# Kernel optimization log

Hardware: AMD Instinct MI355X
Metric: run time of the kernel (lower is better)

The kernel has to match this reference:

```python
import jax, jax.numpy as jnp
import numpy as np

DIM = 1024
DEPTH = 4
VOCAB = 32000
B, N = 2, 2048
DFF = 4096
FG = 0.9  # frac_gradient_state_transition


def setup_inputs() -> dict:
    key = jax.random.key(0)
    ks = jax.random.split(key, 12)
    s = 0.02
    d = DIM
    return {
        "tokens": jax.random.randint(ks[0], (B, N), 0, VOCAB, dtype=jnp.int32),
        "emb": jax.random.normal(ks[1], (VOCAB, d), jnp.float32) * s,
        "g1": jnp.ones((DEPTH, d), jnp.float32),
        "Wqkv": jax.random.normal(ks[2], (DEPTH, d, 3 * d), jnp.float32) * s,
        "Wa": jax.random.normal(ks[3], (DEPTH, d, 2 * d), jnp.float32) * s,
        "ba": jnp.zeros((DEPTH, 2 * d), jnp.float32),
        "Wg": jax.random.normal(ks[4], (DEPTH, d, d), jnp.float32) * s,
        "Wo": jax.random.normal(ks[5], (DEPTH, d, d), jnp.float32) * s,
        "g2": jnp.ones((DEPTH, d), jnp.float32),
        "W1": jax.random.normal(ks[6], (DEPTH, d, DFF), jnp.float32) * s,
        "b1": jnp.zeros((DEPTH, DFF), jnp.float32),
        "W2": jax.random.normal(ks[7], (DEPTH, DFF, d), jnp.float32) * s,
        "b2": jnp.zeros((DEPTH, d), jnp.float32),
        "gf": jnp.ones((d,), jnp.float32),
        "Wl": jax.random.normal(ks[8], (d, VOCAB), jnp.float32) * s,
    }


def _rms(x, g):
    # F.normalize(x, dim=-1) * sqrt(dim) * gamma  (eps=1e-12 like torch)
    nrm = jnp.sqrt(jnp.sum(x * x, axis=-1, keepdims=True))
    return x / jnp.maximum(nrm, 1e-12) * (x.shape[-1] ** 0.5) * g


def _gate_loop(q, k, v, a):
    # q,k,v: (BH, n, 1) real; a: (BH, n, 1) complex
    kv = k[..., :, None] * v[..., None, :]          # (BH, n, 1, 1)
    a = a[..., None]                                 # (BH, n, 1, 1)
    a = jax.nn.sigmoid(jnp.abs(a)) * jnp.exp(1j * jnp.angle(a))  # polar(sigmoid(|a|), angle(a))

    def binop(c1, c2):
        a_i, kv_i = c1
        a_j, kv_j = c2
        return a_j * a_i, a_j.real * kv_i + kv_j

    _, kv = jax.lax.associative_scan(binop, (a, kv), axis=1)
    return jnp.einsum('bnd,bnde->bne', q, kv)        # (BH, n, 1)


def _attn(x, g1, Wqkv, Wa, ba, Wg, Wo):
    b, n, d = x.shape
    h = d  # heads == dim_inner, head dim == 1
    xn = _rms(x, g1)
    q, k, v = jnp.split(xn @ Wqkv, 3, axis=-1)       # each (b, n, d)
    split = lambda t: t.reshape(b, n, h, 1).transpose(0, 2, 1, 3).reshape(b * h, n, 1)
    q, k, v = split(q), split(k), split(v)
    al = (xn @ Wa + ba).reshape(b, n, h, 2).transpose(0, 2, 1, 3).reshape(b * h, n, 1, 2)
    a = al[..., 0] + 1j * al[..., 1]                 # (b*h, n, 1) complex
    a = FG * a + (1.0 - FG) * jax.lax.stop_gradient(a)
    out = _gate_loop(q, k, v, a)                     # (b*h, n, 1)
    out = out.reshape(b, h, n, 1).transpose(0, 2, 1, 3).reshape(b, n, d)
    gates = jax.nn.silu(xn @ Wg)
    return (gates * out) @ Wo


def _ff(x, g2, W1, b1, W2, b2):
    hdn = jax.nn.gelu(_rms(x, g2) @ W1 + b1, approximate=False)
    return hdn @ W2 + b2


def reference(tokens, emb, g1, Wqkv, Wa, ba, Wg, Wo, g2, W1, b1, W2, b2, gf, Wl):
    x = emb[tokens]                                  # (B, N, DIM)
    for i in range(DEPTH):
        x = x + _attn(x, g1[i], Wqkv[i], Wa[i], ba[i], Wg[i], Wo[i])
        x = x + _ff(x, g2[i], W1[i], b1[i], W2[i], b2[i])
    return _rms(x, gf) @ Wl                          # (B, N, VOCAB) logits
```

## Files before the change

### kernel.cpp

```cpp
#include <hip/hip_runtime.h>


typedef float fx4 __attribute__((ext_vector_type(4)));
typedef _Float16 f16x8 __attribute__((ext_vector_type(8)));
typedef _Float16 f16x4 __attribute__((ext_vector_type(4)));

#define AS1 __attribute__((address_space(1)))
#define AS3 __attribute__((address_space(3)))

__global__ __launch_bounds__(256) void transpose_f16_kernel(
    const float* __restrict__ in, _Float16* __restrict__ out,
    int K, int N, size_t ostride)
{
    __shared__ float tile[32][33];
    const int b = blockIdx.z;
    in  += (size_t)b * K * N;
    out += (size_t)b * ostride;
    const int k0 = blockIdx.x * 32, n0 = blockIdx.y * 32;
    const int tr = threadIdx.x >> 3;
    const int tc = (threadIdx.x & 7) * 4;
    fx4 v = *(const fx4*)&in[(size_t)(k0 + tr) * N + n0 + tc];
    tile[tr][tc + 0] = v[0]; tile[tr][tc + 1] = v[1];
    tile[tr][tc + 2] = v[2]; tile[tr][tc + 3] = v[3];
    __syncthreads();
    f16x4 o;
    #pragma unroll
    for (int e = 0; e < 4; ++e) o[e] = (_Float16)tile[tc + e][tr];
    *(f16x4*)&out[(size_t)(n0 + tr) * K + k0 + tc] = o;
}

__device__ __forceinline__ float row_rms_scale(float ss) {
    #pragma unroll
    for (int off = 32; off > 0; off >>= 1) ss += __shfl_down(ss, off, 64);
    __shared__ float wsum[4];
    if ((threadIdx.x & 63) == 0) wsum[threadIdx.x >> 6] = ss;
    __syncthreads();
    const float nrm = sqrtf(wsum[0] + wsum[1] + wsum[2] + wsum[3]);
    return 32.0f / fmaxf(nrm, 1e-12f);
}

__global__ __launch_bounds__(256) void embed_rms_kernel(
    const int* __restrict__ tokens, const float* __restrict__ emb,
    const float* __restrict__ g, float* __restrict__ x, _Float16* __restrict__ xn)
{
    const int row = blockIdx.x;
    const int t = tokens[row];
    const int c = threadIdx.x * 4;
    fx4 v = *(const fx4*)&emb[(size_t)t * 1024 + c];
    *(fx4*)&x[(size_t)row * 1024 + c] = v;
    const float scale = row_rms_scale(v[0]*v[0] + v[1]*v[1] + v[2]*v[2] + v[3]*v[3]);
    fx4 gg = *(const fx4*)&g[c];
    f16x4 o;
    #pragma unroll
    for (int e = 0; e < 4; ++e) o[e] = (_Float16)(v[e] * scale * gg[e]);
    *(f16x4*)&xn[(size_t)row * 1024 + c] = o;
}

__global__ __launch_bounds__(256) void rms_f16_kernel(
    const float* __restrict__ x, const float* __restrict__ g,
    _Float16* __restrict__ outh)
{
    const int row = blockIdx.x;
    const int c = threadIdx.x * 4;
    fx4 v = *(const fx4*)&x[(size_t)row * 1024 + c];
    const float scale = row_rms_scale(v[0]*v[0] + v[1]*v[1] + v[2]*v[2] + v[3]*v[3]);
    fx4 gg = *(const fx4*)&g[c];
    f16x4 o;
    #pragma unroll
    for (int e = 0; e < 4; ++e) o[e] = (_Float16)(v[e] * scale * gg[e]);
    *(f16x4*)&outh[(size_t)row * 1024 + c] = o;
}

__global__ __launch_bounds__(256) void prep_qkv_kernel(
    const float* __restrict__ qkv, float* __restrict__ qT, float* __restrict__ kvT)
{
    __shared__ float tq[32][33], tkv[32][33];
    const int n0 = blockIdx.x * 32, h0 = blockIdx.y * 32, b = blockIdx.z;
    const int tr = threadIdx.x >> 3;
    const int tc = (threadIdx.x & 7) * 4;
    const float* row = qkv + ((size_t)b * 2048 + n0 + tr) * 3072;
    fx4 qv = *(const fx4*)&row[h0 + tc];
    fx4 kv = *(const fx4*)&row[1024 + h0 + tc];
    fx4 vv = *(const fx4*)&row[2048 + h0 + tc];
    #pragma unroll
    for (int e = 0; e < 4; ++e) { tq[tr][tc + e] = qv[e]; tkv[tr][tc + e] = kv[e] * vv[e]; }
    __syncthreads();
    fx4 oq, okv;
    #pragma unroll
    for (int e = 0; e < 4; ++e) { oq[e] = tq[tc + e][tr]; okv[e] = tkv[tc + e][tr]; }
    const size_t ob = ((size_t)b * 1024 + h0 + tr) * 2048 + n0 + tc;
    *(fx4*)&qT[ob] = oq;
    *(fx4*)&kvT[ob] = okv;
}

__global__ __launch_bounds__(256) void prep_a_kernel(
    const float* __restrict__ al, float* __restrict__ aReT, float* __restrict__ aImT)
{
    __shared__ float tre[32][33], tim[32][33];
    const int n0 = blockIdx.x * 32, h0 = blockIdx.y * 32, b = blockIdx.z;
    const int tr = threadIdx.x >> 3;
    const int tcf = (threadIdx.x & 7) * 8;
    const float* row = al + ((size_t)b * 2048 + n0 + tr) * 2048 + 2 * h0;
    fx4 v0 = *(const fx4*)&row[tcf];
    fx4 v1 = *(const fx4*)&row[tcf + 4];
    #pragma unroll
    for (int p = 0; p < 4; ++p) {
        float re = (p < 2) ? v0[2 * p] : v1[2 * (p - 2)];
        float im = (p < 2) ? v0[2 * p + 1] : v1[2 * (p - 2) + 1];
        float r = sqrtf(re * re + im * im);
        float sg = 1.0f / (1.0f + expf(-r));
        float a_re, a_im;
        if (r > 0.0f) { float inv = sg / r; a_re = re * inv; a_im = im * inv; }
        else          { a_re = sg; a_im = 0.0f; }
        tre[tr][tcf / 2 + p] = a_re;
        tim[tr][tcf / 2 + p] = a_im;
    }
    __syncthreads();
    const int tc = (threadIdx.x & 7) * 4;
    fx4 ore, oim;
    #pragma unroll
    for (int e = 0; e < 4; ++e) { ore[e] = tre[tc + e][tr]; oim[e] = tim[tc + e][tr]; }
    const size_t ob = ((size_t)b * 1024 + h0 + tr) * 2048 + n0 + tc;
    *(fx4*)&aReT[ob] = ore;
    *(fx4*)&aImT[ob] = oim;
}

__device__ __forceinline__ int pidx(int i) { return i + (i >> 5); }

__global__ __launch_bounds__(256) void scanT_kernel(
    const float* __restrict__ kvT, const float* __restrict__ aReT,
    const float* __restrict__ aImT, const float* __restrict__ qT,
    float* __restrict__ yT)
{
    const int tid = threadIdx.x;
    const size_t base = (size_t)blockIdx.x * 2048;
    __shared__ float s_re[2048 + 64], s_im[2048 + 64], s_kv[2048 + 64];

    for (int i = tid; i < 512; i += 256) {
        fx4 kv = *(const fx4*)&kvT[base + i * 4];
        fx4 re = *(const fx4*)&aReT[base + i * 4];
        fx4 im = *(const fx4*)&aImT[base + i * 4];
        #pragma unroll
        for (int e = 0; e < 4; ++e) {
            const int j = pidx(i * 4 + e);
            s_kv[j] = kv[e]; s_re[j] = re[e]; s_im[j] = im[e];
        }
    }
    __syncthreads();

    for (int d = 0; d < 11; ++d) {
        const int half = 1 << d, stride = half << 1;
        const int npairs = 2048 >> (d + 1);
        for (int i = tid; i < npairs; i += 256) {
            const int rj = pidx(i * stride + stride - 1);
            const int lj = pidx(i * stride + stride - 1 - half);
            float lre = s_re[lj], lim = s_im[lj], lkv = s_kv[lj];
            float rre = s_re[rj], rim = s_im[rj], rkv = s_kv[rj];
            s_kv[rj] = rre * lkv + rkv;
            s_re[rj] = rre * lre - rim * lim;
            s_im[rj] = rre * lim + rim * lre;
        }
        __syncthreads();
    }
    for (int d = 9; d >= 0; --d) {
        const int w = 1 << d;
        const int nupd = (2048 >> (d + 1)) - 1;
        for (int t = tid; t < nupd; t += 256) {
            const int i = t + 1;
            const int rj = pidx((2 * i + 1) * w - 1);
            const int lj = pidx(2 * i * w - 1);
            float lre = s_re[lj], lim = s_im[lj], lkv = s_kv[lj];
            float rre = s_re[rj], rim = s_im[rj], rkv = s_kv[rj];
            s_kv[rj] = rre * lkv + rkv;
            s_re[rj] = rre * lre - rim * lim;
            s_im[rj] = rre * lim + rim * lre;
        }
        __syncthreads();
    }
    for (int i = tid; i < 512; i += 256) {
        fx4 q = *(const fx4*)&qT[base + i * 4];
        fx4 o;
        #pragma unroll
        for (int e = 0; e < 4; ++e) o[e] = q[e] * s_kv[pidx(i * 4 + e)];
        *(fx4*)&yT[base + i * 4] = o;
    }
}

__global__ __launch_bounds__(256) void gate_kernel(
    const float* __restrict__ G, const float* __restrict__ yT,
    _Float16* __restrict__ gated)
{
    __shared__ float ty[32][33];
    const int n0 = blockIdx.x * 32, h0 = blockIdx.y * 32, b = blockIdx.z;
    const int tr = threadIdx.x >> 3;
    const int tc = (threadIdx.x & 7) * 4;
    fx4 yv = *(const fx4*)&yT[((size_t)b * 1024 + h0 + tr) * 2048 + n0 + tc];
    #pragma unroll
    for (int e = 0; e < 4; ++e) ty[tr][tc + e] = yv[e];
    __syncthreads();
    const size_t grow = ((size_t)b * 2048 + n0 + tr) * 1024 + h0 + tc;
    fx4 gv = *(const fx4*)&G[grow];
    f16x4 o;
    #pragma unroll
    for (int e = 0; e < 4; ++e) {
        const float s = gv[e] / (1.0f + expf(-gv[e]));
        o[e] = (_Float16)(s * ty[tc + e][tr]);
    }
    *(f16x4*)&gated[grow] = o;
}

__global__ __launch_bounds__(256) void combine2_rms_kernel(
    const float* __restrict__ p, const float* __restrict__ bias,
    const float* __restrict__ g, float* __restrict__ x, _Float16* __restrict__ xn)
{
    const int row = blockIdx.x;
    const int c = threadIdx.x * 4;
    const size_t i = (size_t)row * 1024 + c;
    fx4 a = *(const fx4*)&p[i];
    fx4 b = *(const fx4*)&p[i + (size_t)4096 * 1024];
    fx4 xx = *(const fx4*)&x[i];
    fx4 bb = *(const fx4*)&bias[c];
    fx4 o;
    #pragma unroll
    for (int e = 0; e < 4; ++e) o[e] = xx[e] + (a[e] + b[e] + bb[e]);
    *(fx4*)&x[i] = o;
    const float scale = row_rms_scale(o[0]*o[0] + o[1]*o[1] + o[2]*o[2] + o[3]*o[3]);
    fx4 gg = *(const fx4*)&g[c];
    f16x4 oh;
    #pragma unroll
    for (int e = 0; e < 4; ++e) oh[e] = (_Float16)(o[e] * scale * gg[e]);
    *(f16x4*)&xn[i] = oh;
}

template<int EPI, int BM, int BN, int WTM>
__global__ __launch_bounds__((BM / WTM) * (BN / 64) * 64) void gemm_kernel(
    const _Float16* __restrict__ A, const _Float16* __restrict__ Bt,
    const float* __restrict__ bias,
    float* __restrict__ Cf, float* __restrict__ Cf2, float* __restrict__ Cf3,
    _Float16* __restrict__ Ch,
    int M, int N, int K, int Kld)
{
    constexpr int NW      = BN / 64;
    constexpr int THREADS = (BM / WTM) * NW * 64;
    constexpr int M_REP   = WTM / 16;
    __shared__ __align__(16) _Float16 As[BM * 64];
    __shared__ __align__(16) _Float16 Bs[BN * 64];
    const int tid  = threadIdx.x;
    const int lane = tid & 63;
    const int wave = tid >> 6;
    const int bm = blockIdx.x, bn = blockIdx.y;
    const int bz = blockIdx.z;
    const int wm = (wave / NW) * WTM;
    const int wn = (wave % NW) * 64;

    A  += (size_t)bz * K;
    Bt += (size_t)bz * K;
    if (EPI == 0) Cf += (size_t)bz * M * N;

    fx4 acc[M_REP][4] = {};

    const size_t aRow0 = (size_t)bm * BM;
    const size_t bRow0 = (size_t)bn * BN;

    for (int k0 = 0; k0 < K; k0 += 64) {
        constexpr int QA = BM * 8 / THREADS;
        #pragma unroll
        for (int q = 0; q < QA; ++q) {
            const int chunk = q * THREADS + tid;
            const int row = chunk >> 3;
            const int slot = chunk & 7;
            const int gs = slot ^ (row & 7);
            const size_t aoff = (aRow0 + row) * (size_t)Kld + k0 + gs * 8;
            __builtin_amdgcn_global_load_lds((const AS1 void*)(A + aoff),
                (AS3 void*)((char*)As + chunk * 16), 16, 0, 0);
        }
        constexpr int QB = BN * 8 / THREADS;
        #pragma unroll
        for (int q = 0; q < QB; ++q) {
            const int chunk = q * THREADS + tid;
            const int row = chunk >> 3;
            const int slot = chunk & 7;
            const int gs = slot ^ (row & 7);
            const size_t boff = (bRow0 + row) * (size_t)Kld + k0 + gs * 8;
            __builtin_amdgcn_global_load_lds((const AS1 void*)(Bt + boff),
                (AS3 void*)((char*)Bs + chunk * 16), 16, 0, 0);
        }
        __syncthreads();

        #pragma unroll
        for (int kk = 0; kk < 2; ++kk) {
            const int sw = ((kk * 4 + (lane >> 4)) ^ (lane & 7)) * 16;
            f16x8 af[M_REP], bf[4];
            #pragma unroll
            for (int i = 0; i < M_REP; ++i) {
                const int row = wm + i * 16 + (lane & 15);
                af[i] = *(const f16x8*)((const char*)As + row * 128 + sw);
            }
            #pragma unroll
            for (int j = 0; j < 4; ++j) {
                const int row = wn + j * 16 + (lane & 15);
                bf[j] = *(const f16x8*)((const char*)Bs + row * 128 + sw);
            }
            #pragma unroll
            for (int i = 0; i < M_REP; ++i)
                #pragma unroll
                for (int j = 0; j < 4; ++j)
                    acc[i][j] = __builtin_amdgcn_mfma_f32_16x16x32_f16(
                        af[i], bf[j], acc[i][j], 0, 0, 0);
        }
        __syncthreads();
    }

    const int col_l = lane & 15, row_l = (lane >> 4) * 4;
    #pragma unroll
    for (int i = 0; i < M_REP; ++i) {
        #pragma unroll
        for (int j = 0; j < 4; ++j) {
            #pragma unroll
            for (int r = 0; r < 4; ++r) {
                const int row = bm * BM + wm + i * 16 + row_l + r;
                const int col = bn * BN + wn + j * 16 + col_l;
                const float v = acc[i][j][r];
                if (EPI == 0) {
                    Cf[(size_t)row * N + col] = v;
                } else if (EPI == 2) {
                    Cf[(size_t)row * N + col] += v;
                } else if (EPI == 4) {
                    const float t = v + bias[col];
                    const float gelu = 0.5f * t * (1.0f + erff(t * 0.70710678118654752f));
                    Ch[(size_t)row * N + col] = (_Float16)gelu;
                } else if (EPI == 6) {
                    if (col < 3072)      Cf [(size_t)row * 3072 + col] = v;
                    else if (col < 5120) Cf2[(size_t)row * 2048 + (col - 3072)] = v + bias[col - 3072];
                    else                 Cf3[(size_t)row * 1024 + (col - 5120)] = v;
                }
            }
        }
    }
}

extern "C" void kernel_launch(void* const* d_in, const int* in_sizes, int n_in,
                              void* d_out, int out_size, void* d_ws, size_t ws_size,
                              hipStream_t stream)
{
    const int*   tokens = (const int*)d_in[0];
    const float* emb  = (const float*)d_in[1];
    const float* g1   = (const float*)d_in[2];
    const float* Wqkv = (const float*)d_in[3];
    const float* Wa   = (const float*)d_in[4];
    const float* ba   = (const float*)d_in[5];
    const float* Wg   = (const float*)d_in[6];
    const float* Wo   = (const float*)d_in[7];
    const float* g2   = (const float*)d_in[8];
    const float* W1   = (const float*)d_in[9];
    const float* b1   = (const float*)d_in[10];
    const float* W2   = (const float*)d_in[11];
    const float* b2   = (const float*)d_in[12];
    const float* gf   = (const float*)d_in[13];
    const float* Wl   = (const float*)d_in[14];
    float* out = (float*)d_out;

    char* ws = (char*)d_ws;
    size_t off = 0;
    auto take = [&](size_t bytes) {
        char* p = ws + off; off += (bytes + 255) & ~(size_t)255; return p;
    };

    _Float16* wcat = (_Float16*)take((size_t)4 * 6144 * 1024 * 2);
    _Float16* wo   = (_Float16*)take((size_t)4 * 1024 * 1024 * 2);
    _Float16* w1   = (_Float16*)take((size_t)4 * 4096 * 1024 * 2);
    _Float16* w2   = (_Float16*)take((size_t)4 * 1024 * 4096 * 2);
    char*     wlRegion = take((size_t)64 << 20);
    _Float16* wl   = (_Float16*)wlRegion;
    float*    x    = (float*)take((size_t)4096 * 1024 * 4);
    _Float16* xn   = (_Float16*)take((size_t)4096 * 1024 * 2);
    float*    qkvb = (float*)take((size_t)4096 * 3072 * 4);
    float*    alb  = (float*)take((size_t)4096 * 2048 * 4);
    float*    G    = (float*)take((size_t)4096 * 1024 * 4);

    float* qT   = (float*)wlRegion;
    float* kvT  = (float*)(wlRegion + ((size_t)16 << 20));
    float* aReT = (float*)(wlRegion + ((size_t)32 << 20));
    float* aImT = (float*)(wlRegion + ((size_t)48 << 20));
    float*    yT    = alb;
    _Float16* gated = (_Float16*)((char*)alb + ((size_t)16 << 20));
    _Float16* h     = (_Float16*)qkvb;
    float*    part  = alb;

    const dim3 blk(256);

    transpose_f16_kernel<<<dim3(32,  96, 4), blk, 0, stream>>>(Wqkv, wcat,               1024, 3072, (size_t)6144 * 1024);
    transpose_f16_kernel<<<dim3(32,  64, 4), blk, 0, stream>>>(Wa,   wcat + 3072 * 1024, 1024, 2048, (size_t)6144 * 1024);
    transpose_f16_kernel<<<dim3(32,  32, 4), blk, 0, stream>>>(Wg,   wcat + 5120 * 1024, 1024, 1024, (size_t)6144 * 1024);
    transpose_f16_kernel<<<dim3(32,  32, 4), blk, 0, stream>>>(Wo,   wo,  1024, 1024, (size_t)1024 * 1024);
    transpose_f16_kernel<<<dim3(32, 128, 4), blk, 0, stream>>>(W1,   w1,  1024, 4096, (size_t)4096 * 1024);
    transpose_f16_kernel<<<dim3(128, 32, 4), blk, 0, stream>>>(W2,   w2,  4096, 1024, (size_t)1024 * 4096);

    embed_rms_kernel<<<4096, blk, 0, stream>>>(tokens, emb, g1, x, xn);

    for (int i = 0; i < 4; ++i) {
        gemm_kernel<6, 256, 128, 64><<<dim3(16, 48), dim3(512), 0, stream>>>(
            xn, wcat + (size_t)i * 6144 * 1024, ba + i * 2048,
            qkvb, alb, G, nullptr, 4096, 6144, 1024, 1024);
        prep_qkv_kernel<<<dim3(64, 32, 2), blk, 0, stream>>>(qkvb, qT, kvT);
        prep_a_kernel<<<dim3(64, 32, 2), blk, 0, stream>>>(alb, aReT, aImT);
        scanT_kernel<<<2048, blk, 0, stream>>>(kvT, aReT, aImT, qT, yT);
        gate_kernel<<<dim3(64, 32, 2), blk, 0, stream>>>(G, yT, gated);
        gemm_kernel<2, 128, 128, 64><<<dim3(32, 8), blk, 0, stream>>>(
            gated, wo + (size_t)i * 1024 * 1024, nullptr,
            x, nullptr, nullptr, nullptr, 4096, 1024, 1024, 1024);
        rms_f16_kernel<<<4096, blk, 0, stream>>>(x, g2 + i * 1024, xn);
        gemm_kernel<4, 256, 128, 64><<<dim3(16, 32), dim3(512), 0, stream>>>(
            xn, w1 + (size_t)i * 4096 * 1024, b1 + i * 4096,
            nullptr, nullptr, nullptr, h, 4096, 4096, 1024, 1024);
        gemm_kernel<0, 256, 128, 64><<<dim3(16, 8, 2), dim3(512), 0, stream>>>(
            h, w2 + (size_t)i * 1024 * 4096, nullptr,
            part, nullptr, nullptr, nullptr, 4096, 1024, 2048, 4096);
        const float* gnext = (i < 3) ? (g1 + (i + 1) * 1024) : gf;
        combine2_rms_kernel<<<4096, blk, 0, stream>>>(part, b2 + i * 1024, gnext, x, xn);
    }

    transpose_f16_kernel<<<dim3(32, 1000, 1), blk, 0, stream>>>(Wl, wl, 1024, 32000, 0);

    gemm_kernel<0, 256, 128, 64><<<dim3(16, 250), dim3(512), 0, stream>>>(
        xn, wl, nullptr, out, nullptr, nullptr, nullptr, 4096, 32000, 1024, 1024);
}
```

Baseline: 1.627 ms.

## Add 256x256-tile GEMM with 4-stage async LDS pipeline for FF1 and logits

Introduces a new GEMM kernel with 256x256 block tiles, K-step 32, a 4-deep ring of LDS buffers filled by direct global-to-LDS loads with an XOR swizzle, and interleaved barriers that split each K-step into two MFMA halves. It replaces the 256x128 GEMM for the W1 (GELU epilogue) projection and the final vocabulary projection. The larger tile raises arithmetic intensity and halves B-operand reloads, and the deeper prefetch aims to hide global latency. The cost is more LDS (128 KB) and accumulator registers, which limits occupancy to one block per CU, and fewer blocks for the W1 GEMM (256), which may underfill the GPU.

New measurement: 1.797 ms. 1.1x slower.

```diff
diff --git a/kernel.cpp b/kernel.cpp
--- a/kernel.cpp
+++ b/kernel.cpp
@@ -339,6 +339,121 @@
     }
 }
 
+template<int EPI>
+__global__ __launch_bounds__(512) void gemm8_kernel(
+    const _Float16* __restrict__ A, const _Float16* __restrict__ Bt,
+    const float* __restrict__ bias, float* __restrict__ Cf,
+    _Float16* __restrict__ Ch, int M, int N, int K)
+{
+    __shared__ __align__(16) _Float16 As[4][256 * 32];
+    __shared__ __align__(16) _Float16 Bs[4][256 * 32];
+    const int tid = threadIdx.x, lane = tid & 63, wave = tid >> 6;
+    const int bm = blockIdx.x, bn = blockIdx.y;
+    const int wm = (wave >> 2) * 128;
+    const int wn = (wave & 3) * 64;
+    const size_t aRow0 = (size_t)bm * 256;
+    const size_t bRow0 = (size_t)bn * 256;
+
+    fx4 acc[8][4] = {};
+
+    auto stageA = [&](int h) {
+        _Float16* dst = &As[h & 3][0];
+        const int k0 = h * 32;
+        #pragma unroll
+        for (int q = 0; q < 2; ++q) {
+            const int ch = q * 512 + tid;
+            const int line = ch >> 3, cslot = ch & 7;
+            const int u = cslot ^ (line & 7);
+            const int row = line * 2 + (u >> 2);
+            const size_t off = (aRow0 + row) * (size_t)K + k0 + (u & 3) * 8;
+            __builtin_amdgcn_global_load_lds((const AS1 void*)(A + off),
+                (AS3 void*)((char*)dst + ch * 16), 16, 0, 0);
+        }
+    };
+    auto stageB = [&](int h) {
+        _Float16* dst = &Bs[h & 3][0];
+        const int k0 = h * 32;
+        #pragma unroll
+        for (int q = 0; q < 2; ++q) {
+            const int ch = q * 512 + tid;
+            const int line = ch >> 3, cslot = ch & 7;
+            const int u = cslot ^ (line & 7);
+            const int row = line * 2 + (u >> 2);
+            const size_t off = (bRow0 + row) * (size_t)K + k0 + (u & 3) * 8;
+            __builtin_amdgcn_global_load_lds((const AS1 void*)(Bt + off),
+                (AS3 void*)((char*)dst + ch * 16), 16, 0, 0);
+        }
+    };
+    const int g0 = lane >> 4;
+    auto rdA = [&](int slot, int fi) -> f16x8 {
+        const int r = wm + fi * 16 + (lane & 15);
+        const int byte = (r >> 1) * 128 + ((((r & 1) << 2) + g0) ^ ((r >> 1) & 7)) * 16;
+        return *(const f16x8*)((const char*)&As[slot][0] + byte);
+    };
+    auto rdB = [&](int slot, int j) -> f16x8 {
+        const int r = wn + j * 16 + (lane & 15);
+        const int byte = (r >> 1) * 128 + ((((r & 1) << 2) + g0) ^ ((r >> 1) & 7)) * 16;
+        return *(const f16x8*)((const char*)&Bs[slot][0] + byte);
+    };
+
+    stageA(0); stageB(0); stageA(1); stageB(1); stageA(2); stageB(2);
+    asm volatile("s_waitcnt vmcnt(8)" ::: "memory");
+    __builtin_amdgcn_s_barrier();
+
+    const int nH = K >> 5;
+    for (int h = 0; h < nH; ++h) {
+        const int slot = h & 3;
+        f16x8 bf[4];
+        #pragma unroll
+        for (int rh = 0; rh < 2; ++rh) {
+            f16x8 af[4];
+            #pragma unroll
+            for (int i = 0; i < 4; ++i) af[i] = rdA(slot, rh * 4 + i);
+            if (rh == 0) {
+                #pragma unroll
+                for (int j = 0; j < 4; ++j) bf[j] = rdB(slot, j);
+                stageA(h + 3);
+            } else {
+                stageB(h + 3);
+            }
+            __builtin_amdgcn_s_barrier();
+            asm volatile("s_waitcnt lgkmcnt(0)" ::: "memory");
+            __builtin_amdgcn_sched_barrier(0);
+            __builtin_amdgcn_s_setprio(1);
+            #pragma unroll
+            for (int i = 0; i < 4; ++i)
+                #pragma unroll
+                for (int j = 0; j < 4; ++j)
+                    acc[rh * 4 + i][j] = __builtin_amdgcn_mfma_f32_16x16x32_f16(
+                        af[i], bf[j], acc[rh * 4 + i][j], 0, 0, 0);
+            __builtin_amdgcn_s_setprio(0);
+            if (rh == 1) asm volatile("s_waitcnt vmcnt(8)" ::: "memory");
+            __builtin_amdgcn_s_barrier();
+        }
+    }
+
+    const int col_l = lane & 15, row_l = (lane >> 4) * 4;
+    #pragma unroll
+    for (int i = 0; i < 8; ++i) {
+        #pragma unroll
+        for (int j = 0; j < 4; ++j) {
+            #pragma unroll
+            for (int r = 0; r < 4; ++r) {
+                const int row = bm * 256 + wm + i * 16 + row_l + r;
+                const int col = bn * 256 + wn + j * 16 + col_l;
+                const float v = acc[i][j][r];
+                if (EPI == 0) {
+                    Cf[(size_t)row * N + col] = v;
+                } else if (EPI == 4) {
+                    const float t = v + bias[col];
+                    const float gelu = 0.5f * t * (1.0f + erff(t * 0.70710678118654752f));
+                    Ch[(size_t)row * N + col] = (_Float16)gelu;
+                }
+            }
+        }
+    }
+}
+
 extern "C" void kernel_launch(void* const* d_in, const int* in_sizes, int n_in,
                               void* d_out, int out_size, void* d_ws, size_t ws_size,
                               hipStream_t stream)
@@ -410,9 +525,9 @@
             gated, wo + (size_t)i * 1024 * 1024, nullptr,
             x, nullptr, nullptr, nullptr, 4096, 1024, 1024, 1024);
         rms_f16_kernel<<<4096, blk, 0, stream>>>(x, g2 + i * 1024, xn);
-        gemm_kernel<4, 256, 128, 64><<<dim3(16, 32), dim3(512), 0, stream>>>(
+        gemm8_kernel<4><<<dim3(16, 16), dim3(512), 0, stream>>>(
             xn, w1 + (size_t)i * 4096 * 1024, b1 + i * 4096,
-            nullptr, nullptr, nullptr, h, 4096, 4096, 1024, 1024);
+            nullptr, h, 4096, 4096, 1024);
         gemm_kernel<0, 256, 128, 64><<<dim3(16, 8, 2), dim3(512), 0, stream>>>(
             h, w2 + (size_t)i * 1024 * 4096, nullptr,
             part, nullptr, nullptr, nullptr, 4096, 1024, 2048, 4096);
@@ -422,6 +537,6 @@
 
     transpose_f16_kernel<<<dim3(32, 1000, 1), blk, 0, stream>>>(Wl, wl, 1024, 32000, 0);
 
-    gemm_kernel<0, 256, 128, 64><<<dim3(16, 250), dim3(512), 0, stream>>>(
-        xn, wl, nullptr, out, nullptr, nullptr, nullptr, 4096, 32000, 1024, 1024);
-}
+    gemm8_kernel<0><<<dim3(16, 125), dim3(512), 0, stream>>>(
+        xn, wl, nullptr, out, nullptr, 4096, 32000, 1024);
+}
```

## Use triple-buffered direct-to-LDS GEMM for final vocabulary projection

Applied to the files above, without the earlier changes.

Adds a dedicated GEMM kernel for the output logits projection. It uses a 3-slot LDS ring filled by global_load_lds with an XOR-swizzled layout and a K-step of 32, keeping two loads in flight while MFMAs run on the current slot. Raised wave priority around the MFMA block is meant to hide memory latency in the largest GEMM. It drops the generic epilogue and assumes K is a multiple of 32 and that M and N divide the tile.

After: 1.655 ms. No clear change (+1.7%).

```diff
diff --git a/kernel.cpp b/kernel.cpp
--- a/kernel.cpp
+++ b/kernel.cpp
@@ -339,6 +339,89 @@
     }
 }
 
+__global__ __launch_bounds__(512) void gemm_ring3_kernel(
+    const _Float16* __restrict__ A, const _Float16* __restrict__ Bt,
+    float* __restrict__ Cf, int M, int N, int K)
+{
+    __shared__ __align__(16) _Float16 As[3][256 * 32];
+    __shared__ __align__(16) _Float16 Bs[3][128 * 32];
+    const int tid = threadIdx.x, lane = tid & 63, wave = tid >> 6;
+    const int bm = blockIdx.x, bn = blockIdx.y;
+    const int wm = (wave >> 1) * 64, wn = (wave & 1) * 64;
+    const size_t aRow0 = (size_t)bm * 256, bRow0 = (size_t)bn * 128;
+
+    fx4 acc[4][4] = {};
+
+    auto stage = [&](int h) {
+        const int slot = h % 3;
+        const int k0 = h * 32;
+        #pragma unroll
+        for (int q = 0; q < 2; ++q) {
+            const int ch = q * 512 + tid;
+            const int line = ch >> 3;
+            const int u = (ch & 7) ^ (line & 7);
+            const int row = line * 2 + (u >> 2);
+            const size_t off = (aRow0 + row) * (size_t)K + k0 + (u & 3) * 8;
+            __builtin_amdgcn_global_load_lds((const AS1 void*)(A + off),
+                (AS3 void*)((char*)&As[slot][0] + ch * 16), 16, 0, 0);
+        }
+        {
+            const int ch = tid;
+            const int line = ch >> 3;
+            const int u = (ch & 7) ^ (line & 7);
+            const int row = line * 2 + (u >> 2);
+            const size_t off = (bRow0 + row) * (size_t)K + k0 + (u & 3) * 8;
+            __builtin_amdgcn_global_load_lds((const AS1 void*)(Bt + off),
+                (AS3 void*)((char*)&Bs[slot][0] + ch * 16), 16, 0, 0);
+        }
+    };
+    const int g0 = lane >> 4;
+    auto ldoff = [&](int r) -> int {
+        return (r >> 1) * 128 + ((((r & 1) << 2) + g0) ^ ((r >> 1) & 7)) * 16;
+    };
+
+    stage(0); stage(1);
+    asm volatile("s_waitcnt vmcnt(3)" ::: "memory");
+    __builtin_amdgcn_s_barrier();
+
+    const int nH = K >> 5;
+    for (int h = 0; h < nH; ++h) {
+        const int slot = h % 3;
+        f16x8 af[4], bf[4];
+        #pragma unroll
+        for (int i = 0; i < 4; ++i)
+            af[i] = *(const f16x8*)((const char*)&As[slot][0] + ldoff(wm + i * 16 + (lane & 15)));
+        #pragma unroll
+        for (int j = 0; j < 4; ++j)
+            bf[j] = *(const f16x8*)((const char*)&Bs[slot][0] + ldoff(wn + j * 16 + (lane & 15)));
+        stage(h + 2);
+        asm volatile("s_waitcnt lgkmcnt(0)" ::: "memory");
+        __builtin_amdgcn_sched_barrier(0);
+        __builtin_amdgcn_s_setprio(1);
+        #pragma unroll
+        for (int i = 0; i < 4; ++i)
+            #pragma unroll
+            for (int j = 0; j < 4; ++j)
+                acc[i][j] = __builtin_amdgcn_mfma_f32_16x16x32_f16(
+                    af[i], bf[j], acc[i][j], 0, 0, 0);
+        __builtin_amdgcn_s_setprio(0);
+        asm volatile("s_waitcnt vmcnt(3)" ::: "memory");
+        __builtin_amdgcn_s_barrier();
+    }
+
+    const int col_l = lane & 15, row_l = (lane >> 4) * 4;
+    #pragma unroll
+    for (int i = 0; i < 4; ++i)
+        #pragma unroll
+        for (int j = 0; j < 4; ++j)
+            #pragma unroll
+            for (int r = 0; r < 4; ++r) {
+                const int row = bm * 256 + wm + i * 16 + row_l + r;
+                const int col = bn * 128 + wn + j * 16 + col_l;
+                Cf[(size_t)row * N + col] = acc[i][j][r];
+            }
+}
+
 extern "C" void kernel_launch(void* const* d_in, const int* in_sizes, int n_in,
                               void* d_out, int out_size, void* d_ws, size_t ws_size,
                               hipStream_t stream)
@@ -422,6 +505,6 @@
 
     transpose_f16_kernel<<<dim3(32, 1000, 1), blk, 0, stream>>>(Wl, wl, 1024, 32000, 0);
 
-    gemm_kernel<0, 256, 128, 64><<<dim3(16, 250), dim3(512), 0, stream>>>(
-        xn, wl, nullptr, out, nullptr, nullptr, nullptr, 4096, 32000, 1024, 1024);
-}
+    gemm_ring3_kernel<<<dim3(16, 250), dim3(512), 0, stream>>>(
+        xn, wl, out, 4096, 32000, 1024);
+}
```

## Fuse qkv/a prep into QKV GEMM epilogue with interleaved k/v weights

Applied to the files above, without the earlier changes.

Interleaves the k and v weight rows when transposing Wqkv so adjacent GEMM output columns hold k and v for the same head. The EPI 6 GEMM epilogue then forms k*v and the sigmoid-polar a values using a lane shuffle, and writes q, kv, aRe and aIm directly in the head-major transposed layout the scan expects. This removes the prep_qkv and prep_a kernels and the round trip of qkv and a-logits through global memory. In exchange, the epilogue stores become strided column-wise fx4 writes, which may coalesce poorly.

New measurement: 1.563 ms. 3.9% less time.

```diff
diff --git a/kernel.cpp b/kernel.cpp
--- a/kernel.cpp
+++ b/kernel.cpp
@@ -29,6 +29,30 @@
     *(f16x4*)&out[(size_t)(n0 + tr) * K + k0 + tc] = o;
 }
 
+__global__ __launch_bounds__(256) void transpose_qkv_kernel(
+    const float* __restrict__ in, _Float16* __restrict__ out)
+{
+    __shared__ float tile[32][33];
+    const int b = blockIdx.z;
+    in  += (size_t)b * 1024 * 3072;
+    out += (size_t)b * 6144 * 1024;
+    const int k0 = blockIdx.x * 32, n0 = blockIdx.y * 32;
+    const int tr = threadIdx.x >> 3;
+    const int tc = (threadIdx.x & 7) * 4;
+    fx4 v = *(const fx4*)&in[(size_t)(k0 + tr) * 3072 + n0 + tc];
+    tile[tr][tc + 0] = v[0]; tile[tr][tc + 1] = v[1];
+    tile[tr][tc + 2] = v[2]; tile[tr][tc + 3] = v[3];
+    __syncthreads();
+    const int col = n0 + tr;
+    const int orow = (col < 1024) ? col
+                   : (col < 2048) ? 1024 + 2 * (col - 1024)
+                                  : 1024 + 2 * (col - 2048) + 1;
+    f16x4 o;
+    #pragma unroll
+    for (int e = 0; e < 4; ++e) o[e] = (_Float16)tile[tc + e][tr];
+    *(f16x4*)&out[(size_t)orow * 1024 + k0 + tc] = o;
+}
+
 __device__ __forceinline__ float row_rms_scale(float ss) {
     #pragma unroll
     for (int off = 32; off > 0; off >>= 1) ss += __shfl_down(ss, off, 64);
@@ -69,60 +93,6 @@
     #pragma unroll
     for (int e = 0; e < 4; ++e) o[e] = (_Float16)(v[e] * scale * gg[e]);
     *(f16x4*)&outh[(size_t)row * 1024 + c] = o;
-}
-
-__global__ __launch_bounds__(256) void prep_qkv_kernel(
-    const float* __restrict__ qkv, float* __restrict__ qT, float* __restrict__ kvT)
-{
-    __shared__ float tq[32][33], tkv[32][33];
-    const int n0 = blockIdx.x * 32, h0 = blockIdx.y * 32, b = blockIdx.z;
-    const int tr = threadIdx.x >> 3;
-    const int tc = (threadIdx.x & 7) * 4;
-    const float* row = qkv + ((size_t)b * 2048 + n0 + tr) * 3072;
-    fx4 qv = *(const fx4*)&row[h0 + tc];
-    fx4 kv = *(const fx4*)&row[1024 + h0 + tc];
-    fx4 vv = *(const fx4*)&row[2048 + h0 + tc];
-    #pragma unroll
-    for (int e = 0; e < 4; ++e) { tq[tr][tc + e] = qv[e]; tkv[tr][tc + e] = kv[e] * vv[e]; }
-    __syncthreads();
-    fx4 oq, okv;
-    #pragma unroll
-    for (int e = 0; e < 4; ++e) { oq[e] = tq[tc + e][tr]; okv[e] = tkv[tc + e][tr]; }
-    const size_t ob = ((size_t)b * 1024 + h0 + tr) * 2048 + n0 + tc;
-    *(fx4*)&qT[ob] = oq;
-    *(fx4*)&kvT[ob] = okv;
-}
-
-__global__ __launch_bounds__(256) void prep_a_kernel(
-    const float* __restrict__ al, float* __restrict__ aReT, float* __restrict__ aImT)
-{
-    __shared__ float tre[32][33], tim[32][33];
-    const int n0 = blockIdx.x * 32, h0 = blockIdx.y * 32, b = blockIdx.z;
-    const int tr = threadIdx.x >> 3;
-    const int tcf = (threadIdx.x & 7) * 8;
-    const float* row = al + ((size_t)b * 2048 + n0 + tr) * 2048 + 2 * h0;
-    fx4 v0 = *(const fx4*)&row[tcf];
-    fx4 v1 = *(const fx4*)&row[tcf + 4];
-    #pragma unroll
-    for (int p = 0; p < 4; ++p) {
-        float re = (p < 2) ? v0[2 * p] : v1[2 * (p - 2)];
-        float im = (p < 2) ? v0[2 * p + 1] : v1[2 * (p - 2) + 1];
-        float r = sqrtf(re * re + im * im);
-        float sg = 1.0f / (1.0f + expf(-r));
-        float a_re, a_im;
-        if (r > 0.0f) { float inv = sg / r; a_re = re * inv; a_im = im * inv; }
-        else          { a_re = sg; a_im = 0.0f; }
-        tre[tr][tcf / 2 + p] = a_re;
-        tim[tr][tcf / 2 + p] = a_im;
-    }
-    __syncthreads();
-    const int tc = (threadIdx.x & 7) * 4;
-    fx4 ore, oim;
-    #pragma unroll
-    for (int e = 0; e < 4; ++e) { ore[e] = tre[tc + e][tr]; oim[e] = tim[tc + e][tr]; }
-    const size_t ob = ((size_t)b * 1024 + h0 + tr) * 2048 + n0 + tc;
-    *(fx4*)&aReT[ob] = ore;
-    *(fx4*)&aImT[ob] = oim;
 }
 
 __device__ __forceinline__ int pidx(int i) { return i + (i >> 5); }
@@ -237,6 +207,7 @@
     const _Float16* __restrict__ A, const _Float16* __restrict__ Bt,
     const float* __restrict__ bias,
     float* __restrict__ Cf, float* __restrict__ Cf2, float* __restrict__ Cf3,
+    float* __restrict__ aRe, float* __restrict__ aIm,
     _Float16* __restrict__ Ch,
     int M, int N, int K, int Kld)
 {
@@ -316,23 +287,69 @@
     for (int i = 0; i < M_REP; ++i) {
         #pragma unroll
         for (int j = 0; j < 4; ++j) {
-            #pragma unroll
-            for (int r = 0; r < 4; ++r) {
-                const int row = bm * BM + wm + i * 16 + row_l + r;
-                const int col = bn * BN + wn + j * 16 + col_l;
-                const float v = acc[i][j][r];
-                if (EPI == 0) {
-                    Cf[(size_t)row * N + col] = v;
-                } else if (EPI == 2) {
-                    Cf[(size_t)row * N + col] += v;
-                } else if (EPI == 4) {
-                    const float t = v + bias[col];
-                    const float gelu = 0.5f * t * (1.0f + erff(t * 0.70710678118654752f));
-                    Ch[(size_t)row * N + col] = (_Float16)gelu;
-                } else if (EPI == 6) {
-                    if (col < 3072)      Cf [(size_t)row * 3072 + col] = v;
-                    else if (col < 5120) Cf2[(size_t)row * 2048 + (col - 3072)] = v + bias[col - 3072];
-                    else                 Cf3[(size_t)row * 1024 + (col - 5120)] = v;
+            if (EPI == 6) {
+                const int col  = bn * BN + wn + j * 16 + col_l;
+                const int row0 = bm * BM + wm + i * 16 + row_l;
+                const int b = row0 >> 11;
+                const int n = row0 & 2047;
+                if (col < 1024) {
+                    *(fx4*)&Cf[((size_t)b * 1024 + col) * 2048 + n] = acc[i][j];
+                } else if (col < 3072) {
+                    fx4 partner;
+                    #pragma unroll
+                    for (int e = 0; e < 4; ++e)
+                        partner[e] = __shfl_xor(acc[i][j][e], 1, 64);
+                    if ((col & 1) == 0) {
+                        fx4 kv;
+                        #pragma unroll
+                        for (int e = 0; e < 4; ++e) kv[e] = acc[i][j][e] * partner[e];
+                        const int hh = (col - 1024) >> 1;
+                        *(fx4*)&Cf2[((size_t)b * 1024 + hh) * 2048 + n] = kv;
+                    }
+                } else if (col < 5120) {
+                    fx4 my;
+                    #pragma unroll
+                    for (int e = 0; e < 4; ++e) my[e] = acc[i][j][e] + bias[col - 3072];
+                    fx4 partner;
+                    #pragma unroll
+                    for (int e = 0; e < 4; ++e)
+                        partner[e] = __shfl_xor(my[e], 1, 64);
+                    const bool isRe = (col & 1) == 0;
+                    const int hh = (col - 3072) >> 1;
+                    fx4 o;
+                    #pragma unroll
+                    for (int e = 0; e < 4; ++e) {
+                        const float re = isRe ? my[e] : partner[e];
+                        const float im = isRe ? partner[e] : my[e];
+                        const float r = sqrtf(re * re + im * im);
+                        const float sg = 1.0f / (1.0f + expf(-r));
+                        float a_re, a_im;
+                        if (r > 0.0f) { const float inv = sg / r; a_re = re * inv; a_im = im * inv; }
+                        else          { a_re = sg; a_im = 0.0f; }
+                        o[e] = isRe ? a_re : a_im;
+                    }
+                    if (isRe) *(fx4*)&aRe[((size_t)b * 1024 + hh) * 2048 + n] = o;
+                    else      *(fx4*)&aIm[((size_t)b * 1024 + hh) * 2048 + n] = o;
+                } else {
+                    #pragma unroll
+                    for (int r = 0; r < 4; ++r)
+                        Cf3[(size_t)(row0 + r) * 1024 + (col - 5120)] = acc[i][j][r];
+                }
+            } else {
+                #pragma unroll
+                for (int r = 0; r < 4; ++r) {
+                    const int row = bm * BM + wm + i * 16 + row_l + r;
+                    const int col = bn * BN + wn + j * 16 + col_l;
+                    const float v = acc[i][j][r];
+                    if (EPI == 0) {
+                        Cf[(size_t)row * N + col] = v;
+                    } else if (EPI == 2) {
+                        Cf[(size_t)row * N + col] += v;
+                    } else if (EPI == 4) {
+                        const float t = v + bias[col];
+                        const float gelu = 0.5f * t * (1.0f + erff(t * 0.70710678118654752f));
+                        Ch[(size_t)row * N + col] = (_Float16)gelu;
+                    }
                 }
             }
         }
@@ -389,7 +406,7 @@
 
     const dim3 blk(256);
 
-    transpose_f16_kernel<<<dim3(32,  96, 4), blk, 0, stream>>>(Wqkv, wcat,               1024, 3072, (size_t)6144 * 1024);
+    transpose_qkv_kernel<<<dim3(32, 96, 4), blk, 0, stream>>>(Wqkv, wcat);
     transpose_f16_kernel<<<dim3(32,  64, 4), blk, 0, stream>>>(Wa,   wcat + 3072 * 1024, 1024, 2048, (size_t)6144 * 1024);
     transpose_f16_kernel<<<dim3(32,  32, 4), blk, 0, stream>>>(Wg,   wcat + 5120 * 1024, 1024, 1024, (size_t)6144 * 1024);
     transpose_f16_kernel<<<dim3(32,  32, 4), blk, 0, stream>>>(Wo,   wo,  1024, 1024, (size_t)1024 * 1024);
@@ -401,21 +418,19 @@
     for (int i = 0; i < 4; ++i) {
         gemm_kernel<6, 256, 128, 64><<<dim3(16, 48), dim3(512), 0, stream>>>(
             xn, wcat + (size_t)i * 6144 * 1024, ba + i * 2048,
-            qkvb, alb, G, nullptr, 4096, 6144, 1024, 1024);
-        prep_qkv_kernel<<<dim3(64, 32, 2), blk, 0, stream>>>(qkvb, qT, kvT);
-        prep_a_kernel<<<dim3(64, 32, 2), blk, 0, stream>>>(alb, aReT, aImT);
+            qT, kvT, G, aReT, aImT, nullptr, 4096, 6144, 1024, 1024);
         scanT_kernel<<<2048, blk, 0, stream>>>(kvT, aReT, aImT, qT, yT);
         gate_kernel<<<dim3(64, 32, 2), blk, 0, stream>>>(G, yT, gated);
         gemm_kernel<2, 128, 128, 64><<<dim3(32, 8), blk, 0, stream>>>(
             gated, wo + (size_t)i * 1024 * 1024, nullptr,
-            x, nullptr, nullptr, nullptr, 4096, 1024, 1024, 1024);
+            x, nullptr, nullptr, nullptr, nullptr, nullptr, 4096, 1024, 1024, 1024);
         rms_f16_kernel<<<4096, blk, 0, stream>>>(x, g2 + i * 1024, xn);
         gemm_kernel<4, 256, 128, 64><<<dim3(16, 32), dim3(512), 0, stream>>>(
             xn, w1 + (size_t)i * 4096 * 1024, b1 + i * 4096,
-            nullptr, nullptr, nullptr, h, 4096, 4096, 1024, 1024);
+            nullptr, nullptr, nullptr, nullptr, nullptr, h, 4096, 4096, 1024, 1024);
         gemm_kernel<0, 256, 128, 64><<<dim3(16, 8, 2), dim3(512), 0, stream>>>(
             h, w2 + (size_t)i * 1024 * 4096, nullptr,
-            part, nullptr, nullptr, nullptr, 4096, 1024, 2048, 4096);
+            part, nullptr, nullptr, nullptr, nullptr, nullptr, 4096, 1024, 2048, 4096);
         const float* gnext = (i < 3) ? (g1 + (i + 1) * 1024) : gf;
         combine2_rms_kernel<<<4096, blk, 0, stream>>>(part, b2 + i * 1024, gnext, x, xn);
     }
@@ -423,5 +438,6 @@
     transpose_f16_kernel<<<dim3(32, 1000, 1), blk, 0, stream>>>(Wl, wl, 1024, 32000, 0);
 
     gemm_kernel<0, 256, 128, 64><<<dim3(16, 250), dim3(512), 0, stream>>>(
-        xn, wl, nullptr, out, nullptr, nullptr, nullptr, 4096, 32000, 1024, 1024);
-}
+        xn, wl, nullptr, out, nullptr, nullptr, nullptr, nullptr, nullptr,
+        4096, 32000, 1024, 1024);
+}
```
